# Kernel optimization log

Hardware: AMD Instinct MI355X
Metric: run time of the kernel (lower is better)

The kernel has to match this reference:

```python
import jax, jax.numpy as jnp
import numpy as np

B, T, C = 16, 4096, 256


def setup_inputs() -> dict:
    key = jax.random.key(0)
    kx, kl = jax.random.split(key)
    x = jax.random.normal(kx, (B, T, C), dtype=jnp.float32)
    lengths = jax.random.randint(kl, (B,), T // 2, T + 1)  # valid lengths per sample
    pool_ranges = lengths  # region to pool over; k <= pool_range guaranteed by layer/total_layers choice
    return {
        "x": x,
        "lengths": lengths,
        "pool_ranges": pool_ranges,
        "top_k": 4,
        "layer": 1,
        "total_layers": 4,
    }


def _pool_one(xb, k, pool_range):
    # xb: [T, C]; keep, per column independently, the k largest values among the
    # first pool_range rows, preserving original row order (torch kmax_pooling).
    Trows, Ccols = xb.shape
    valid = jnp.arange(Trows) < pool_range            # [T]
    vals = jnp.where(valid[:, None], xb, -jnp.inf)    # mask invalid rows to rank last
    order = jnp.argsort(-vals, axis=0)                # descending order per column
    rank = jnp.argsort(order, axis=0)                 # inverse permutation = rank of each row
    keep = (rank < k) & valid[:, None]                # [T, C] which entries survive
    pos = jnp.cumsum(keep.astype(jnp.int32), axis=0) - 1  # compacted output row per column
    idx = jnp.where(keep, pos, Trows)                 # dropped entries -> dummy row Trows
    cols = jnp.arange(Ccols)[None, :]
    out = jnp.zeros((Trows + 1, Ccols), xb.dtype).at[idx, cols].set(
        jnp.where(keep, xb, jnp.zeros((), xb.dtype))
    )
    return out[:-1]                                   # [T, C]; rows >= k are zero padding


def reference(x, lengths, pool_ranges, top_k, layer, total_layers):
    # pool_target = max(top_k, ceil((total_layers - layer)/total_layers * length))
    num = total_layers - layer
    k = jnp.maximum(top_k, (num * lengths + total_layers - 1) // total_layers)
    k = jnp.minimum(k, pool_ranges)  # topk requires k <= available rows
    results = jax.vmap(_pool_one)(x, k, pool_ranges)  # [B, T, C], zero-padded past k_i
    pool_result_ranges = k
    return results, pool_result_ranges
```

## Files before the change

### kernel.cpp

```cpp
#include <hip/hip_runtime.h>
#include <stdint.h>


constexpr int T_ROWS = 4096;
constexpr int C_COLS = 256;
constexpr int NBATCH = 16;
constexpr int SBLOCK = 512;
constexpr int EPT    = T_ROWS / SBLOCK;
constexpr int NCOL   = 4;
constexpr int NSUB   = 4;
constexpr int HPAD   = 8;
constexpr int HSTRIDE = 256 * NSUB + HPAD;
constexpr int NGROUP = C_COLS / NCOL;
constexpr int NBLK   = NBATCH * NGROUP;
constexpr size_t NTOT = (size_t)NBATCH * T_ROWS * C_COLS;

__device__ __forceinline__ int compute_k(const int* lengths, const int* pool_ranges,
                                         const int* p_top_k, const int* p_layer,
                                         const int* p_total, int b, int* pr_out)
{
    int pr = pool_ranges[b];
    pr = pr < 0 ? 0 : (pr > T_ROWS ? T_ROWS : pr);
    const int len   = lengths[b];
    const int top_k = p_top_k[0];
    const int tot   = p_total[0];
    const int num   = tot - p_layer[0];
    int k = (num * len + tot - 1) / tot;
    if (k < top_k) k = top_k;
    if (k > pr)    k = pr;
    *pr_out = pr;
    return k;
}

template<int MODE>
__global__ __launch_bounds__(SBLOCK)
void kmax_select_kernel(const float* __restrict__ x,
                        const int*   __restrict__ lengths,
                        const int*   __restrict__ pool_ranges,
                        const int*   __restrict__ p_top_k,
                        const int*   __restrict__ p_layer,
                        const int*   __restrict__ p_total,
                        float*       __restrict__ out,
                        float*       __restrict__ ws)
{
    __shared__ uint32_t hist[NCOL * HSTRIDE];
    __shared__ uint32_t wsum[SBLOCK / 64][NCOL];
    __shared__ uint32_t sh_sel[NCOL], sh_rem[NCOL];

    const int bid  = blockIdx.x;
    const int lin  = (bid & 7) * (NBLK / 8) + (bid >> 3);
    const int b    = lin / NGROUP;
    const int cg   = lin % NGROUP;
    const int c0   = cg * NCOL;
    const int t    = threadIdx.x;
    const int lane = t & 63;
    const int wid  = t >> 6;

    int pr;
    const int k = compute_k(lengths, pool_ranges, p_top_k, p_layer, p_total, b, &pr);

    const int base_row = t * EPT;
    int nv = pr - base_row;
    nv = nv < 0 ? 0 : (nv > EPT ? EPT : nv);

    const size_t colbase = (size_t)b * T_ROWS * C_COLS + (size_t)c0;

    uint32_t u[EPT][NCOL];
    #pragma unroll
    for (int i = 0; i < EPT; ++i) {
        const float4 v = *reinterpret_cast<const float4*>(
            x + colbase + (size_t)(base_row + i) * C_COLS);
        const uint32_t w[4] = {__float_as_uint(v.x), __float_as_uint(v.y),
                               __float_as_uint(v.z), __float_as_uint(v.w)};
        const bool valid = (i < nv);
        #pragma unroll
        for (int j = 0; j < NCOL; ++j) {
            u[i][j] = valid ? (w[j] ^ ((w[j] >> 31) ? 0xFFFFFFFFu : 0x80000000u))
                            : 0u;
            asm("" : "+v"(u[i][j]));
        }
    }

    uint32_t prefix[NCOL] = {0u, 0u, 0u, 0u};
    uint32_t rem[NCOL];
    #pragma unroll
    for (int j = 0; j < NCOL; ++j) rem[j] = (uint32_t)k;

    if (k > 0) {
        uint32_t pmask = 0u;
        const uint32_t sub = (uint32_t)(t & (NSUB - 1));
        for (int pass = 0; pass < 4; ++pass) {
            const int shift = 24 - 8 * pass;
            for (int z = t; z < NCOL * HSTRIDE; z += SBLOCK) hist[z] = 0u;
            __syncthreads();
            #pragma unroll
            for (int j = 0; j < NCOL; ++j) {
                #pragma unroll
                for (int i = 0; i < EPT; ++i) {
                    if (i < nv) {
                        const uint32_t ui = u[i][j];
                        if ((ui & pmask) == prefix[j])
                            atomicAdd(&hist[j * HSTRIDE +
                                            ((ui >> shift) & 255u) * NSUB + sub], 1u);
                    }
                }
            }
            __syncthreads();
            if (wid < NCOL) {
                const int j = wid;
                uint32_t c4[4], loc[4], s = 0;
                #pragma unroll
                for (int q = 0; q < 4; ++q) {
                    const int bin = 255 - 4 * lane - q;
                    uint32_t cnt = 0;
                    #pragma unroll
                    for (int z = 0; z < NSUB; ++z)
                        cnt += hist[j * HSTRIDE + bin * NSUB + z];
                    c4[q]  = cnt;
                    loc[q] = s;
                    s += cnt;
                }
                uint32_t incl = s;
                #pragma unroll
                for (int off = 1; off < 64; off <<= 1) {
                    const uint32_t nb = __shfl_up(incl, (unsigned)off, 64);
                    if (lane >= off) incl += nb;
                }
                const uint32_t gexcl = incl - s;
                const uint32_t rj = rem[j];
                #pragma unroll
                for (int q = 0; q < 4; ++q) {
                    const uint32_t sbb = gexcl + loc[q];
                    if (sbb < rj && sbb + c4[q] >= rj) {
                        sh_sel[j] = (uint32_t)(255 - 4 * lane - q);
                        sh_rem[j] = rj - sbb;
                    }
                }
            }
            __syncthreads();
            #pragma unroll
            for (int j = 0; j < NCOL; ++j) {
                prefix[j] |= sh_sel[j] << shift;
                rem[j]     = sh_rem[j];
            }
            pmask |= 0xFFu << shift;
        }

        uint32_t mine[NCOL], incl[NCOL];
        #pragma unroll
        for (int j = 0; j < NCOL; ++j) {
            uint32_t gt = 0, eq = 0;
            #pragma unroll
            for (int i = 0; i < EPT; ++i) {
                if (i < nv) {
                    gt += (u[i][j] > prefix[j]) ? 1u : 0u;
                    eq += (u[i][j] == prefix[j]) ? 1u : 0u;
                }
            }
            mine[j] = (gt << 16) | eq;
            uint32_t v = mine[j];
            #pragma unroll
            for (int off = 1; off < 64; off <<= 1) {
                const uint32_t nb = __shfl_up(v, (unsigned)off, 64);
                if (lane >= off) v += nb;
            }
            incl[j] = v;
            if (lane == 63) wsum[wid][j] = v;
        }
        __syncthreads();
        #pragma unroll
        for (int j = 0; j < NCOL; ++j) {
            uint32_t woff = 0;
            for (int w = 0; w < wid; ++w) woff += wsum[w][j];
            const uint32_t excl = incl[j] + woff - mine[j];
            uint32_t g = excl >> 16;
            uint32_t e = excl & 0xFFFFu;
            const uint32_t th = prefix[j], tn = rem[j];
            #pragma unroll
            for (int i = 0; i < EPT; ++i) {
                if (i < nv) {
                    const uint32_t ui = u[i][j];
                    const bool isgt = ui > th;
                    const bool iseq = (ui == th);
                    if (isgt || (iseq && e < tn)) {
                        const uint32_t pos = g + (e < tn ? e : tn);
                        const uint32_t bits =
                            ui ^ ((ui >> 31) ? 0x80000000u : 0xFFFFFFFFu);
                        if (MODE == 0) {
                            ws[(size_t)lin * (T_ROWS * NCOL) +
                               (size_t)pos * NCOL + (size_t)j] = __uint_as_float(bits);
                        } else {
                            out[colbase + (size_t)pos * C_COLS + (size_t)j] =
                                __uint_as_float(bits);
                        }
                    }
                    g += isgt ? 1u : 0u;
                    e += iseq ? 1u : 0u;
                }
            }
        }
    }

    if (MODE == 1) {
        for (int r = k + t; r < T_ROWS; r += SBLOCK) {
            const float4 z = make_float4(0.f, 0.f, 0.f, 0.f);
            *reinterpret_cast<float4*>(out + colbase + (size_t)r * C_COLS) = z;
        }
    }

    if (cg == 0 && t == 0)
        out[NTOT + (size_t)b] = (float)k;
}

constexpr int TBLOCK = 256;

__global__ __launch_bounds__(TBLOCK)
void kmax_transpose_kernel(const float* __restrict__ ws,
                           const int*   __restrict__ lengths,
                           const int*   __restrict__ pool_ranges,
                           const int*   __restrict__ p_top_k,
                           const int*   __restrict__ p_layer,
                           const int*   __restrict__ p_total,
                           float*       __restrict__ out)
{
    extern __shared__ float4 tile_s[];

    const int bid  = blockIdx.x;
    const int b    = bid >> 6;
    const int tile = bid & 63;
    const int pos0 = tile * 64;

    int pr;
    const int k = compute_k(lengths, pool_ranges, p_top_k, p_layer, p_total, b, &pr);

    const int t = threadIdx.x;
    const int w = t >> 6;
    const int l = t & 63;
    const float4 z4 = make_float4(0.f, 0.f, 0.f, 0.f);
    float4* out4 = reinterpret_cast<float4*>(out);

    if (pos0 < k) {
        const float4* ws4 = reinterpret_cast<const float4*>(ws);
        #pragma unroll
        for (int cgi = 0; cgi < 16; ++cgi) {
            const int cg = cgi * 4 + w;
            tile_s[cg * 64 + (l ^ cg)] =
                ws4[(size_t)(b * NGROUP + cg) * T_ROWS + (size_t)(pos0 + l)];
        }
        __syncthreads();
        #pragma unroll
        for (int it = 0; it < 16; ++it) {
            const int idx = it * TBLOCK + t;
            const int row = idx >> 6;
            const int cq  = idx & 63;
            const int pos = pos0 + row;
            const float4 v = (pos < k) ? tile_s[cq * 64 + (row ^ cq)] : z4;
            out4[((size_t)b * T_ROWS + (size_t)pos) * (C_COLS / 4) + (size_t)cq] = v;
        }
    } else {
        #pragma unroll
        for (int it = 0; it < 16; ++it) {
            const int idx = it * TBLOCK + t;
            const int row = idx >> 6;
            const int cq  = idx & 63;
            out4[((size_t)b * T_ROWS + (size_t)(pos0 + row)) * (C_COLS / 4) +
                 (size_t)cq] = z4;
        }
    }
}

extern "C" void kernel_launch(void* const* d_in, const int* in_sizes, int n_in,
                              void* d_out, int out_size, void* d_ws, size_t ws_size,
                              hipStream_t stream)
{
    const float* x            = (const float*)d_in[0];
    const int*   lengths      = (const int*)d_in[1];
    const int*   pool_ranges  = (const int*)d_in[2];
    const int*   top_k        = (const int*)d_in[3];
    const int*   layer        = (const int*)d_in[4];
    const int*   total_layers = (const int*)d_in[5];
    float*       out          = (float*)d_out;
    float*       ws           = (float*)d_ws;

    const size_t ws_need = (size_t)NBLK * T_ROWS * NCOL * sizeof(float);

    if (ws_size >= ws_need) {
        hipLaunchKernelGGL(kmax_select_kernel<0>, dim3(NBLK), dim3(SBLOCK), 0, stream,
                           x, lengths, pool_ranges, top_k, layer, total_layers, out, ws);
        hipLaunchKernelGGL(kmax_transpose_kernel, dim3(NBLK), dim3(TBLOCK), 65536, stream,
                           ws, lengths, pool_ranges, top_k, layer, total_layers, out);
    } else {
        hipLaunchKernelGGL(kmax_select_kernel<1>, dim3(NBLK), dim3(SBLOCK), 0, stream,
                           x, lengths, pool_ranges, top_k, layer, total_layers, out, ws);
    }
}
```

Baseline: 112.3 us.

## Assign one wavefront per column with LDS-staged transpose and ballot-based compaction

```diff
diff --git a/kernel.cpp b/kernel.cpp
--- a/kernel.cpp
+++ b/kernel.cpp
@@ -5,14 +5,15 @@
 constexpr int T_ROWS = 4096;
 constexpr int C_COLS = 256;
 constexpr int NBATCH = 16;
-constexpr int SBLOCK = 512;
-constexpr int EPT    = T_ROWS / SBLOCK;
-constexpr int NCOL   = 4;
-constexpr int NSUB   = 4;
-constexpr int HPAD   = 8;
-constexpr int HSTRIDE = 256 * NSUB + HPAD;
-constexpr int NGROUP = C_COLS / NCOL;
-constexpr int NBLK   = NBATCH * NGROUP;
+constexpr int SBLOCK = 1024;
+constexpr int SWAVES = 16;
+constexpr int NCHUNK = 8;
+constexpr int CROWS  = 512;
+constexpr int CPAD   = 17;
+constexpr int EPL    = 64;
+constexpr int NSUB   = 2;
+constexpr int NGB    = C_COLS / SWAVES;
+constexpr int NBLK   = NBATCH * NGB;
 constexpr size_t NTOT = (size_t)NBATCH * T_ROWS * C_COLS;
 
 __device__ __forceinline__ int compute_k(const int* lengths, const int* pool_ranges,
@@ -33,7 +34,7 @@
 }
 
 template<int MODE>
-__global__ __launch_bounds__(SBLOCK)
+__global__ __launch_bounds__(SBLOCK, 4)
 void kmax_select_kernel(const float* __restrict__ x,
                         const int*   __restrict__ lengths,
                         const int*   __restrict__ pool_ranges,
@@ -43,172 +44,139 @@
                         float*       __restrict__ out,
                         float*       __restrict__ ws)
 {
-    __shared__ uint32_t hist[NCOL * HSTRIDE];
-    __shared__ uint32_t wsum[SBLOCK / 64][NCOL];
-    __shared__ uint32_t sh_sel[NCOL], sh_rem[NCOL];
-
-    const int bid  = blockIdx.x;
-    const int lin  = (bid & 7) * (NBLK / 8) + (bid >> 3);
-    const int b    = lin / NGROUP;
-    const int cg   = lin % NGROUP;
-    const int c0   = cg * NCOL;
+    __shared__ float    stage[2][CROWS][CPAD];
+    __shared__ uint32_t hist[SWAVES][256 * NSUB];
+
     const int t    = threadIdx.x;
     const int lane = t & 63;
     const int wid  = t >> 6;
+    const int bid  = blockIdx.x;
+    const int b    = bid >> 4;
+    const int cgrp = bid & 15;
+    const int c0   = cgrp * 16;
+    const int c    = c0 + wid;
 
     int pr;
     const int k = compute_k(lengths, pool_ranges, p_top_k, p_layer, p_total, b, &pr);
 
-    const int base_row = t * EPT;
-    int nv = pr - base_row;
-    nv = nv < 0 ? 0 : (nv > EPT ? EPT : nv);
-
-    const size_t colbase = (size_t)b * T_ROWS * C_COLS + (size_t)c0;
-
-    uint32_t u[EPT][NCOL];
+    const int rq = t >> 2;
+    const int q  = t & 3;
+    const float* xb = x + (size_t)b * T_ROWS * C_COLS + (size_t)c0 + (size_t)(q * 4);
+    float4 ga[NCHUNK], gb[NCHUNK];
     #pragma unroll
-    for (int i = 0; i < EPT; ++i) {
-        const float4 v = *reinterpret_cast<const float4*>(
-            x + colbase + (size_t)(base_row + i) * C_COLS);
-        const uint32_t w[4] = {__float_as_uint(v.x), __float_as_uint(v.y),
-                               __float_as_uint(v.z), __float_as_uint(v.w)};
-        const bool valid = (i < nv);
-        #pragma unroll
-        for (int j = 0; j < NCOL; ++j) {
-            u[i][j] = valid ? (w[j] ^ ((w[j] >> 31) ? 0xFFFFFFFFu : 0x80000000u))
-                            : 0u;
-            asm("" : "+v"(u[i][j]));
-        }
-    }
-
-    uint32_t prefix[NCOL] = {0u, 0u, 0u, 0u};
-    uint32_t rem[NCOL];
+    for (int ci = 0; ci < NCHUNK; ++ci) {
+        ga[ci] = *reinterpret_cast<const float4*>(xb + (size_t)(ci * CROWS + rq) * C_COLS);
+        gb[ci] = *reinterpret_cast<const float4*>(xb + (size_t)(ci * CROWS + 256 + rq) * C_COLS);
+    }
+
+    uint32_t u[EPL];
     #pragma unroll
-    for (int j = 0; j < NCOL; ++j) rem[j] = (uint32_t)k;
-
+    for (int ci = 0; ci < NCHUNK; ++ci) {
+        const int buf = ci & 1;
+        stage[buf][rq      ][q * 4 + 0] = ga[ci].x;
+        stage[buf][rq      ][q * 4 + 1] = ga[ci].y;
+        stage[buf][rq      ][q * 4 + 2] = ga[ci].z;
+        stage[buf][rq      ][q * 4 + 3] = ga[ci].w;
+        stage[buf][rq + 256][q * 4 + 0] = gb[ci].x;
+        stage[buf][rq + 256][q * 4 + 1] = gb[ci].y;
+        stage[buf][rq + 256][q * 4 + 2] = gb[ci].z;
+        stage[buf][rq + 256][q * 4 + 3] = gb[ci].w;
+        __syncthreads();
+        #pragma unroll
+        for (int mm = 0; mm < 8; ++mm) {
+            const int m = ci * 8 + mm;
+            const uint32_t w = __float_as_uint(stage[buf][mm * 64 + lane][wid]);
+            const uint32_t key = w ^ ((w >> 31) ? 0xFFFFFFFFu : 0x80000000u);
+            u[m] = ((m * 64 + lane) < pr) ? key : 0u;
+            asm("" : "+v"(u[m]));
+        }
+    }
+
+    uint32_t prefix = 0u, pmask = 0u, rem = (uint32_t)k;
     if (k > 0) {
-        uint32_t pmask = 0u;
-        const uint32_t sub = (uint32_t)(t & (NSUB - 1));
         for (int pass = 0; pass < 4; ++pass) {
             const int shift = 24 - 8 * pass;
-            for (int z = t; z < NCOL * HSTRIDE; z += SBLOCK) hist[z] = 0u;
-            __syncthreads();
-            #pragma unroll
-            for (int j = 0; j < NCOL; ++j) {
+            #pragma unroll
+            for (int z = 0; z < (256 * NSUB) / 64; ++z)
+                hist[wid][z * 64 + lane] = 0u;
+            #pragma unroll
+            for (int m = 0; m < EPL; ++m) {
+                const uint32_t ui = u[m];
+                if ((ui & pmask) == prefix)
+                    atomicAdd(&hist[wid][((ui >> shift) & 255u) * NSUB + (lane & (NSUB - 1))], 1u);
+            }
+            uint32_t c4[4], loc[4], s = 0;
+            #pragma unroll
+            for (int qq = 0; qq < 4; ++qq) {
+                const int bin = 255 - (lane * 4 + qq);
+                uint32_t cnt = 0;
                 #pragma unroll
-                for (int i = 0; i < EPT; ++i) {
-                    if (i < nv) {
-                        const uint32_t ui = u[i][j];
-                        if ((ui & pmask) == prefix[j])
-                            atomicAdd(&hist[j * HSTRIDE +
-                                            ((ui >> shift) & 255u) * NSUB + sub], 1u);
-                    }
+                for (int z = 0; z < NSUB; ++z) cnt += hist[wid][bin * NSUB + z];
+                c4[qq] = cnt; loc[qq] = s; s += cnt;
+            }
+            uint32_t incl = s;
+            #pragma unroll
+            for (int off = 1; off < 64; off <<= 1) {
+                const uint32_t nb = __shfl_up(incl, (unsigned)off, 64);
+                if (lane >= off) incl += nb;
+            }
+            const uint32_t gexcl = incl - s;
+            uint32_t sel = 0, nrem = 0;
+            bool found = false;
+            #pragma unroll
+            for (int qq = 0; qq < 4; ++qq) {
+                const uint32_t sbb = gexcl + loc[qq];
+                if (sbb < rem && sbb + c4[qq] >= rem) {
+                    sel  = (uint32_t)(255 - (lane * 4 + qq));
+                    nrem = rem - sbb;
+                    found = true;
                 }
             }
-            __syncthreads();
-            if (wid < NCOL) {
-                const int j = wid;
-                uint32_t c4[4], loc[4], s = 0;
-                #pragma unroll
-                for (int q = 0; q < 4; ++q) {
-                    const int bin = 255 - 4 * lane - q;
-                    uint32_t cnt = 0;
-                    #pragma unroll
-                    for (int z = 0; z < NSUB; ++z)
-                        cnt += hist[j * HSTRIDE + bin * NSUB + z];
-                    c4[q]  = cnt;
-                    loc[q] = s;
-                    s += cnt;
-                }
-                uint32_t incl = s;
-                #pragma unroll
-                for (int off = 1; off < 64; off <<= 1) {
-                    const uint32_t nb = __shfl_up(incl, (unsigned)off, 64);
-                    if (lane >= off) incl += nb;
-                }
-                const uint32_t gexcl = incl - s;
-                const uint32_t rj = rem[j];
-                #pragma unroll
-                for (int q = 0; q < 4; ++q) {
-                    const uint32_t sbb = gexcl + loc[q];
-                    if (sbb < rj && sbb + c4[q] >= rj) {
-                        sh_sel[j] = (uint32_t)(255 - 4 * lane - q);
-                        sh_rem[j] = rj - sbb;
-                    }
-                }
-            }
-            __syncthreads();
-            #pragma unroll
-            for (int j = 0; j < NCOL; ++j) {
-                prefix[j] |= sh_sel[j] << shift;
-                rem[j]     = sh_rem[j];
-            }
-            pmask |= 0xFFu << shift;
-        }
-
-        uint32_t mine[NCOL], incl[NCOL];
-        #pragma unroll
-        for (int j = 0; j < NCOL; ++j) {
-            uint32_t gt = 0, eq = 0;
-            #pragma unroll
-            for (int i = 0; i < EPT; ++i) {
-                if (i < nv) {
-                    gt += (u[i][j] > prefix[j]) ? 1u : 0u;
-                    eq += (u[i][j] == prefix[j]) ? 1u : 0u;
-                }
-            }
-            mine[j] = (gt << 16) | eq;
-            uint32_t v = mine[j];
-            #pragma unroll
-            for (int off = 1; off < 64; off <<= 1) {
-                const uint32_t nb = __shfl_up(v, (unsigned)off, 64);
-                if (lane >= off) v += nb;
-            }
-            incl[j] = v;
-            if (lane == 63) wsum[wid][j] = v;
-        }
-        __syncthreads();
-        #pragma unroll
-        for (int j = 0; j < NCOL; ++j) {
-            uint32_t woff = 0;
-            for (int w = 0; w < wid; ++w) woff += wsum[w][j];
-            const uint32_t excl = incl[j] + woff - mine[j];
-            uint32_t g = excl >> 16;
-            uint32_t e = excl & 0xFFFFu;
-            const uint32_t th = prefix[j], tn = rem[j];
-            #pragma unroll
-            for (int i = 0; i < EPT; ++i) {
-                if (i < nv) {
-                    const uint32_t ui = u[i][j];
-                    const bool isgt = ui > th;
-                    const bool iseq = (ui == th);
-                    if (isgt || (iseq && e < tn)) {
-                        const uint32_t pos = g + (e < tn ? e : tn);
-                        const uint32_t bits =
-                            ui ^ ((ui >> 31) ? 0x80000000u : 0xFFFFFFFFu);
-                        if (MODE == 0) {
-                            ws[(size_t)lin * (T_ROWS * NCOL) +
-                               (size_t)pos * NCOL + (size_t)j] = __uint_as_float(bits);
-                        } else {
-                            out[colbase + (size_t)pos * C_COLS + (size_t)j] =
-                                __uint_as_float(bits);
-                        }
-                    }
-                    g += isgt ? 1u : 0u;
-                    e += iseq ? 1u : 0u;
-                }
-            }
+            const unsigned long long fm = __ballot(found);
+            const int src = __ffsll((unsigned long long)fm) - 1;
+            sel  = __shfl(sel,  src, 64);
+            nrem = __shfl(nrem, src, 64);
+            prefix |= sel << shift;
+            pmask  |= 0xFFu << shift;
+            rem = nrem;
+        }
+
+        const uint32_t th = prefix, tn = rem;
+        const unsigned long long ltm = (1ull << lane) - 1ull;
+        uint32_t G = 0, E = 0;
+        const size_t wsbase  = (size_t)(b * 64 + (c >> 2)) * (size_t)(T_ROWS * 4) + (size_t)(c & 3);
+        const size_t outbase = (size_t)b * T_ROWS * C_COLS + (size_t)c;
+        #pragma unroll
+        for (int m = 0; m < EPL; ++m) {
+            const int row = m * 64 + lane;
+            const uint32_t ui = u[m];
+            const bool v    = row < pr;
+            const bool mygt = v && (ui > th);
+            const bool myeq = v && (ui == th);
+            const unsigned long long gm = __ballot(mygt);
+            const unsigned long long em = __ballot(myeq);
+            const uint32_t my_g = G + (uint32_t)__popcll(gm & ltm);
+            const uint32_t my_e = E + (uint32_t)__popcll(em & ltm);
+            if (mygt || (myeq && my_e < tn)) {
+                const uint32_t pos  = my_g + (my_e < tn ? my_e : tn);
+                const uint32_t bits = ui ^ ((ui >> 31) ? 0x80000000u : 0xFFFFFFFFu);
+                if (MODE == 0)
+                    ws[wsbase + (size_t)pos * 4] = __uint_as_float(bits);
+                else
+                    out[outbase + (size_t)pos * C_COLS] = __uint_as_float(bits);
+            }
+            G += (uint32_t)__popcll(gm);
+            E += (uint32_t)__popcll(em);
         }
     }
 
     if (MODE == 1) {
-        for (int r = k + t; r < T_ROWS; r += SBLOCK) {
-            const float4 z = make_float4(0.f, 0.f, 0.f, 0.f);
-            *reinterpret_cast<float4*>(out + colbase + (size_t)r * C_COLS) = z;
-        }
-    }
-
-    if (cg == 0 && t == 0)
+        const size_t outbase = (size_t)b * T_ROWS * C_COLS + (size_t)c;
+        for (int r = k + lane; r < T_ROWS; r += 64)
+            out[outbase + (size_t)r * C_COLS] = 0.f;
+    }
+
+    if (cgrp == 0 && t == 0)
         out[NTOT + (size_t)b] = (float)k;
 }
 
@@ -245,7 +213,7 @@
         for (int cgi = 0; cgi < 16; ++cgi) {
             const int cg = cgi * 4 + w;
             tile_s[cg * 64 + (l ^ cg)] =
-                ws4[(size_t)(b * NGROUP + cg) * T_ROWS + (size_t)(pos0 + l)];
+                ws4[(size_t)(b * 64 + cg) * T_ROWS + (size_t)(pos0 + l)];
         }
         __syncthreads();
         #pragma unroll
@@ -282,12 +250,12 @@
     float*       out          = (float*)d_out;
     float*       ws           = (float*)d_ws;
 
-    const size_t ws_need = (size_t)NBLK * T_ROWS * NCOL * sizeof(float);
+    const size_t ws_need = (size_t)NBATCH * 64 * T_ROWS * 4 * sizeof(float);
 
     if (ws_size >= ws_need) {
         hipLaunchKernelGGL(kmax_select_kernel<0>, dim3(NBLK), dim3(SBLOCK), 0, stream,
                            x, lengths, pool_ranges, top_k, layer, total_layers, out, ws);
-        hipLaunchKernelGGL(kmax_transpose_kernel, dim3(NBLK), dim3(TBLOCK), 65536, stream,
+        hipLaunchKernelGGL(kmax_transpose_kernel, dim3(NBATCH * 64), dim3(TBLOCK), 65536, stream,
                            ws, lengths, pool_ranges, top_k, layer, total_layers, out);
     } else {
         hipLaunchKernelGGL(kmax_select_kernel<1>, dim3(NBLK), dim3(SBLOCK), 0, stream,
```

New measurement: 92.27 us. 1.22x faster.
